# Performance work log

Measured on AMD Instinct MI355X. Metric: run time of the kernel, lower is better.

## Reference

```python
import jax, jax.numpy as jnp
import numpy as np

WINDOW_SIZE = 11
C1 = 0.01 ** 2
C2 = 0.03 ** 2


def _box_filter(x, ws):
    # x: [B,1,H,W]; uniform box filter, zero padding (== torch conv2d pad=ws//2)
    k = jnp.full((1, 1, ws, ws), 1.0 / (ws * ws), dtype=x.dtype)
    pad = ws // 2
    return jax.lax.conv_general_dilated(
        x, k, window_strides=(1, 1), padding=[(pad, pad), (pad, pad)],
        dimension_numbers=('NCHW', 'OIHW', 'NCHW'))


def setup_inputs() -> dict:
    key = jax.random.key(0)
    k1, k2 = jax.random.split(key)
    img1 = jax.random.uniform(k1, (64, 1, 512, 512), dtype=jnp.float32)
    img2 = jax.random.uniform(k2, (64, 1, 512, 512), dtype=jnp.float32)
    return {"img1": img1, "img2": img2}


def reference(img1, img2):
    ws = WINDOW_SIZE
    mu1 = _box_filter(img1, ws)
    mu2 = _box_filter(img2, ws)
    mu1_sq = mu1 * mu1
    mu2_sq = mu2 * mu2
    mu1_mu2 = mu1 * mu2
    sigma1_sq = _box_filter(img1 * img1, ws) - mu1_sq
    sigma2_sq = _box_filter(img2 * img2, ws) - mu2_sq
    sigma12 = _box_filter(img1 * img2, ws) - mu1_mu2
    ssim_map = ((2 * mu1_mu2 + C1) * (2 * sigma12 + C2)) / (
        (mu1_sq + mu2_sq + C1) * (sigma1_sq + sigma2_sq + C2))
    return 1.0 - jnp.mean(ssim_map)
```

## Files before the change

### kernel.cpp

```cpp
#include <hip/hip_runtime.h>


#define IMG_H 512
#define IMG_W 512
#define N_IMG 64
#define STRIP 16
#define NTHREADS 128
#define SSZ 528
#define QSZ 132
#define ROWSZ (SSZ + QSZ)

__global__ __launch_bounds__(NTHREADS) void ssim_kernel(const float* __restrict__ img1,
                                                        const float* __restrict__ img2,
                                                        float* __restrict__ ws) {
    __shared__ __align__(16) float V[2][4][ROWSZ];
    __shared__ float wsum[2];
    const int t = threadIdx.x;
    const int b = blockIdx.y;
    const int r0 = blockIdx.x * STRIP;
    const float* __restrict__ p1 = img1 + (size_t)b * (IMG_H * IMG_W);
    const float* __restrict__ p2 = img2 + (size_t)b * (IMG_H * IMG_W);

    for (int i = t; i < 2 * 4 * ROWSZ; i += NTHREADS) (&V[0][0][0])[i] = 0.0f;

    const int c4 = 4 * t;
    float cs[4][4];
#pragma unroll
    for (int ch = 0; ch < 4; ++ch)
#pragma unroll
        for (int j = 0; j < 4; ++j) cs[ch][j] = 0.0f;

    auto addrow = [&](int r) {
        float4 x = *(const float4*)(p1 + (size_t)r * IMG_W + c4);
        float4 y = *(const float4*)(p2 + (size_t)r * IMG_W + c4);
        float xs[4] = {x.x, x.y, x.z, x.w}, ys[4] = {y.x, y.y, y.z, y.w};
#pragma unroll
        for (int j = 0; j < 4; ++j) {
            float u = xs[j] + ys[j], v = xs[j] - ys[j];
            cs[0][j] += u;                  cs[1][j] += v;
            cs[2][j] = fmaf(u, u, cs[2][j]); cs[3][j] = fmaf(v, v, cs[3][j]);
        }
    };

    float4 pax, pay, psx, psy;
    auto prefetch = [&](int rn) {
        if (rn >= r0 + STRIP) return;
        const int ra = rn + 5, rs = rn - 6;
        if (ra < IMG_H) {
            pax = *(const float4*)(p1 + (size_t)ra * IMG_W + c4);
            pay = *(const float4*)(p2 + (size_t)ra * IMG_W + c4);
        }
        if (rs >= 0) {
            psx = *(const float4*)(p1 + (size_t)rs * IMG_W + c4);
            psy = *(const float4*)(p2 + (size_t)rs * IMG_W + c4);
        }
    };
    auto consume = [&](int rn) {
        const int ra = rn + 5, rs = rn - 6;
        if (ra < IMG_H) {
            float xs[4] = {pax.x, pax.y, pax.z, pax.w};
            float ys[4] = {pay.x, pay.y, pay.z, pay.w};
#pragma unroll
            for (int j = 0; j < 4; ++j) {
                float u = xs[j] + ys[j], v = xs[j] - ys[j];
                cs[0][j] += u;                  cs[1][j] += v;
                cs[2][j] = fmaf(u, u, cs[2][j]); cs[3][j] = fmaf(v, v, cs[3][j]);
            }
        }
        if (rs >= 0) {
            float xs[4] = {psx.x, psx.y, psx.z, psx.w};
            float ys[4] = {psy.x, psy.y, psy.z, psy.w};
#pragma unroll
            for (int j = 0; j < 4; ++j) {
                float u = xs[j] + ys[j], v = xs[j] - ys[j];
                cs[0][j] -= u;                  cs[1][j] -= v;
                cs[2][j] = fmaf(-u, u, cs[2][j]); cs[3][j] = fmaf(-v, v, cs[3][j]);
            }
        }
    };
    auto writeSQ = [&](int p) {
#pragma unroll
        for (int ch = 0; ch < 4; ++ch) {
            *(float4*)&V[p][ch][8 + c4] =
                make_float4(cs[ch][0], cs[ch][1], cs[ch][2], cs[ch][3]);
            V[p][ch][SSZ + 2 + t] = (cs[ch][0] + cs[ch][1]) + (cs[ch][2] + cs[ch][3]);
        }
    };

    int offS[4][3], offQ[4][2];
#pragma unroll
    for (int k = 0; k < 4; ++k) {
        const int c = t + 128 * k;
        const int rho = c & 3;
        int e0, e1, e2;
        if (rho == 0)      { e0 = -5; e1 =  4; e2 =  5; }
        else if (rho == 1) { e0 =  3; e1 =  4; e2 =  5; }
        else if (rho == 2) { e0 = -5; e1 = -4; e2 = -3; }
        else               { e0 = -5; e1 = -4; e2 =  5; }
        offS[k][0] = c + 8 + e0; offS[k][1] = c + 8 + e1; offS[k][2] = c + 8 + e2;
        const int mlo = (c >> 2) + ((rho < 2) ? -1 : 0);
        offQ[k][0] = SSZ + 2 + mlo; offQ[k][1] = SSZ + 3 + mlo;
    }

    {
        int rlo = r0 - 5; if (rlo < 0) rlo = 0;
        const int rhi = r0 + 5;
        for (int r = rlo; r <= rhi; ++r) addrow(r);
    }
    __syncthreads();
    writeSQ(0);
    prefetch(r0 + 1);
    __syncthreads();

    constexpr float inv  = 1.0f / 121.0f;
    constexpr float inv2 = 0.5f / 121.0f;
    constexpr float C1c = 0.01f * 0.01f;
    constexpr float C2c = 0.03f * 0.03f;
    float acc = 0.0f;

    auto hphase = [&](int p) {
        const float* __restrict__ Vf = &V[p][0][0];
#pragma unroll
        for (int k = 0; k < 4; ++k) {
            float W[4];
#pragma unroll
            for (int ch = 0; ch < 4; ++ch) {
                const int base = ch * ROWSZ;
                W[ch] = ((Vf[base + offS[k][0]] + Vf[base + offS[k][1]]) +
                         (Vf[base + offS[k][2]] + Vf[base + offQ[k][0]])) +
                        Vf[base + offQ[k][1]];
            }
            float mu_u = W[0] * inv, mu_v = W[1] * inv;
            float uu = mu_u * mu_u, vv = mu_v * mu_v;
            float P = 0.5f * (uu + vv);
            float M = 0.5f * (uu - vv);
            float A = fmaf(W[2] + W[3], inv2, -P);
            float B = fmaf(W[2] - W[3], inv2, -M);
            float num = (M + C1c) * (B + C2c);
            float den = (P + C1c) * (A + C2c);
            acc += __fdividef(num, den);
        }
    };

    for (int i = 0; i < STRIP - 1; ++i) {
        hphase(i & 1);
        consume(r0 + i + 1);
        prefetch(r0 + i + 2);
        writeSQ((i + 1) & 1);
        __syncthreads();
    }
    hphase((STRIP - 1) & 1);

#pragma unroll
    for (int off = 32; off > 0; off >>= 1) acc += __shfl_down(acc, off);
    if ((t & 63) == 0) wsum[t >> 6] = acc;
    __syncthreads();
    if (t == 0) atomicAdd(ws, wsum[0] + wsum[1]);
}

__global__ void ssim_finalize(const float* __restrict__ ws, float* __restrict__ out) {
    constexpr float inv_n = 1.0f / (float)((size_t)N_IMG * IMG_H * IMG_W);
    out[0] = 1.0f - ws[0] * inv_n;
}

extern "C" void kernel_launch(void* const* d_in, const int* in_sizes, int n_in,
                              void* d_out, int out_size, void* d_ws, size_t ws_size,
                              hipStream_t stream) {
    const float* img1 = (const float*)d_in[0];
    const float* img2 = (const float*)d_in[1];
    float* out = (float*)d_out;
    float* ws = (float*)d_ws;

    hipMemsetAsync(ws, 0, sizeof(float), stream);

    dim3 grid(IMG_H / STRIP, N_IMG);
    ssim_kernel<<<grid, NTHREADS, 0, stream>>>(img1, img2, ws);
    ssim_finalize<<<1, 1, 0, stream>>>(ws, out);
}
```

Measured before the change: 191.8 us.

## Use single-wavefront blocks with one LDS buffer and no block barriers

Shrinks each block to one 64-thread wavefront that covers the full 512-column row, with each thread owning two float4 column groups. Halves the strip height and drops the double-buffered LDS. It also removes every __syncthreads, relying on in-wavefront ordering of LDS writes and reads, and does the final reduction with a single atomic per wave. The aim is to cut barrier stalls and raise occupancy through more, smaller blocks. In exchange, the shorter strips reload more halo rows per output row, and correctness now depends on wavefront-synchronous LDS ordering.

Result: slower. 642.4 us (+235.0%).

```diff
diff --git a/kernel.cpp b/kernel.cpp
--- a/kernel.cpp
+++ b/kernel.cpp
@@ -4,35 +4,33 @@
 #define IMG_H 512
 #define IMG_W 512
 #define N_IMG 64
-#define STRIP 16
-#define NTHREADS 128
+#define STRIP 8
+#define NTHREADS 64
 #define SSZ 528
 #define QSZ 132
 #define ROWSZ (SSZ + QSZ)
 
-__global__ __launch_bounds__(NTHREADS) void ssim_kernel(const float* __restrict__ img1,
-                                                        const float* __restrict__ img2,
-                                                        float* __restrict__ ws) {
-    __shared__ __align__(16) float V[2][4][ROWSZ];
-    __shared__ float wsum[2];
+__global__ __launch_bounds__(NTHREADS, 4) void ssim_kernel(const float* __restrict__ img1,
+                                                           const float* __restrict__ img2,
+                                                           float* __restrict__ ws) {
+    __shared__ __align__(16) float V[4][ROWSZ];
     const int t = threadIdx.x;
     const int b = blockIdx.y;
     const int r0 = blockIdx.x * STRIP;
     const float* __restrict__ p1 = img1 + (size_t)b * (IMG_H * IMG_W);
     const float* __restrict__ p2 = img2 + (size_t)b * (IMG_H * IMG_W);
 
-    for (int i = t; i < 2 * 4 * ROWSZ; i += NTHREADS) (&V[0][0][0])[i] = 0.0f;
+    for (int i = t; i < 4 * ROWSZ; i += NTHREADS) (&V[0][0])[i] = 0.0f;
 
-    const int c4 = 4 * t;
-    float cs[4][4];
+    const int c4a = 4 * t;
+    const int c4b = 4 * t + 256;
+    float csA[4][4], csB[4][4];
 #pragma unroll
     for (int ch = 0; ch < 4; ++ch)
 #pragma unroll
-        for (int j = 0; j < 4; ++j) cs[ch][j] = 0.0f;
+        for (int j = 0; j < 4; ++j) { csA[ch][j] = 0.0f; csB[ch][j] = 0.0f; }
 
-    auto addrow = [&](int r) {
-        float4 x = *(const float4*)(p1 + (size_t)r * IMG_W + c4);
-        float4 y = *(const float4*)(p2 + (size_t)r * IMG_W + c4);
+    auto addQ = [&](float (&cs)[4][4], float4 x, float4 y) {
         float xs[4] = {x.x, x.y, x.z, x.w}, ys[4] = {y.x, y.y, y.z, y.w};
 #pragma unroll
         for (int j = 0; j < 4; ++j) {
@@ -41,94 +39,93 @@
             cs[2][j] = fmaf(u, u, cs[2][j]); cs[3][j] = fmaf(v, v, cs[3][j]);
         }
     };
+    auto subQ = [&](float (&cs)[4][4], float4 x, float4 y) {
+        float xs[4] = {x.x, x.y, x.z, x.w}, ys[4] = {y.x, y.y, y.z, y.w};
+#pragma unroll
+        for (int j = 0; j < 4; ++j) {
+            float u = xs[j] + ys[j], v = xs[j] - ys[j];
+            cs[0][j] -= u;                  cs[1][j] -= v;
+            cs[2][j] = fmaf(-u, u, cs[2][j]); cs[3][j] = fmaf(-v, v, cs[3][j]);
+        }
+    };
 
-    float4 pax, pay, psx, psy;
+#pragma unroll
+    for (int dr = -5; dr <= 5; ++dr) {
+        const int r = r0 + dr;
+        if (r >= 0) {
+            float4 xa = *(const float4*)(p1 + (size_t)r * IMG_W + c4a);
+            float4 ya = *(const float4*)(p2 + (size_t)r * IMG_W + c4a);
+            float4 xb = *(const float4*)(p1 + (size_t)r * IMG_W + c4b);
+            float4 yb = *(const float4*)(p2 + (size_t)r * IMG_W + c4b);
+            addQ(csA, xa, ya); addQ(csB, xb, yb);
+        }
+    }
+
+    float4 paxA, payA, paxB, payB, psxA, psyA, psxB, psyB;
     auto prefetch = [&](int rn) {
         if (rn >= r0 + STRIP) return;
         const int ra = rn + 5, rs = rn - 6;
         if (ra < IMG_H) {
-            pax = *(const float4*)(p1 + (size_t)ra * IMG_W + c4);
-            pay = *(const float4*)(p2 + (size_t)ra * IMG_W + c4);
+            paxA = *(const float4*)(p1 + (size_t)ra * IMG_W + c4a);
+            payA = *(const float4*)(p2 + (size_t)ra * IMG_W + c4a);
+            paxB = *(const float4*)(p1 + (size_t)ra * IMG_W + c4b);
+            payB = *(const float4*)(p2 + (size_t)ra * IMG_W + c4b);
         }
         if (rs >= 0) {
-            psx = *(const float4*)(p1 + (size_t)rs * IMG_W + c4);
-            psy = *(const float4*)(p2 + (size_t)rs * IMG_W + c4);
+            psxA = *(const float4*)(p1 + (size_t)rs * IMG_W + c4a);
+            psyA = *(const float4*)(p2 + (size_t)rs * IMG_W + c4a);
+            psxB = *(const float4*)(p1 + (size_t)rs * IMG_W + c4b);
+            psyB = *(const float4*)(p2 + (size_t)rs * IMG_W + c4b);
         }
     };
     auto consume = [&](int rn) {
         const int ra = rn + 5, rs = rn - 6;
-        if (ra < IMG_H) {
-            float xs[4] = {pax.x, pax.y, pax.z, pax.w};
-            float ys[4] = {pay.x, pay.y, pay.z, pay.w};
-#pragma unroll
-            for (int j = 0; j < 4; ++j) {
-                float u = xs[j] + ys[j], v = xs[j] - ys[j];
-                cs[0][j] += u;                  cs[1][j] += v;
-                cs[2][j] = fmaf(u, u, cs[2][j]); cs[3][j] = fmaf(v, v, cs[3][j]);
-            }
-        }
-        if (rs >= 0) {
-            float xs[4] = {psx.x, psx.y, psx.z, psx.w};
-            float ys[4] = {psy.x, psy.y, psy.z, psy.w};
-#pragma unroll
-            for (int j = 0; j < 4; ++j) {
-                float u = xs[j] + ys[j], v = xs[j] - ys[j];
-                cs[0][j] -= u;                  cs[1][j] -= v;
-                cs[2][j] = fmaf(-u, u, cs[2][j]); cs[3][j] = fmaf(-v, v, cs[3][j]);
-            }
-        }
+        if (ra < IMG_H) { addQ(csA, paxA, payA); addQ(csB, paxB, payB); }
+        if (rs >= 0)    { subQ(csA, psxA, psyA); subQ(csB, psxB, psyB); }
     };
-    auto writeSQ = [&](int p) {
+
+    auto writeSQ = [&]() {
 #pragma unroll
         for (int ch = 0; ch < 4; ++ch) {
-            *(float4*)&V[p][ch][8 + c4] =
-                make_float4(cs[ch][0], cs[ch][1], cs[ch][2], cs[ch][3]);
-            V[p][ch][SSZ + 2 + t] = (cs[ch][0] + cs[ch][1]) + (cs[ch][2] + cs[ch][3]);
+            *(float4*)&V[ch][8 + c4a] =
+                make_float4(csA[ch][0], csA[ch][1], csA[ch][2], csA[ch][3]);
+            *(float4*)&V[ch][8 + c4b] =
+                make_float4(csB[ch][0], csB[ch][1], csB[ch][2], csB[ch][3]);
+            V[ch][SSZ + 2 + t]      = (csA[ch][0] + csA[ch][1]) + (csA[ch][2] + csA[ch][3]);
+            V[ch][SSZ + 2 + 64 + t] = (csB[ch][0] + csB[ch][1]) + (csB[ch][2] + csB[ch][3]);
         }
     };
 
-    int offS[4][3], offQ[4][2];
-#pragma unroll
-    for (int k = 0; k < 4; ++k) {
-        const int c = t + 128 * k;
-        const int rho = c & 3;
+    int sOff[3], qOff[2];
+    {
+        const int rho = t & 3;
         int e0, e1, e2;
         if (rho == 0)      { e0 = -5; e1 =  4; e2 =  5; }
         else if (rho == 1) { e0 =  3; e1 =  4; e2 =  5; }
         else if (rho == 2) { e0 = -5; e1 = -4; e2 = -3; }
         else               { e0 = -5; e1 = -4; e2 =  5; }
-        offS[k][0] = c + 8 + e0; offS[k][1] = c + 8 + e1; offS[k][2] = c + 8 + e2;
-        const int mlo = (c >> 2) + ((rho < 2) ? -1 : 0);
-        offQ[k][0] = SSZ + 2 + mlo; offQ[k][1] = SSZ + 3 + mlo;
+        sOff[0] = t + 8 + e0; sOff[1] = t + 8 + e1; sOff[2] = t + 8 + e2;
+        const int mlo = (t >> 2) + ((rho < 2) ? -1 : 0);
+        qOff[0] = SSZ + 2 + mlo; qOff[1] = SSZ + 3 + mlo;
     }
-
-    {
-        int rlo = r0 - 5; if (rlo < 0) rlo = 0;
-        const int rhi = r0 + 5;
-        for (int r = rlo; r <= rhi; ++r) addrow(r);
-    }
-    __syncthreads();
-    writeSQ(0);
-    prefetch(r0 + 1);
-    __syncthreads();
 
     constexpr float inv  = 1.0f / 121.0f;
     constexpr float inv2 = 0.5f / 121.0f;
     constexpr float C1c = 0.01f * 0.01f;
     constexpr float C2c = 0.03f * 0.03f;
     float acc = 0.0f;
+    const float* __restrict__ Vf = &V[0][0];
 
-    auto hphase = [&](int p) {
-        const float* __restrict__ Vf = &V[p][0][0];
+    auto hphase = [&]() {
 #pragma unroll
-        for (int k = 0; k < 4; ++k) {
+        for (int k = 0; k < 8; ++k) {
             float W[4];
 #pragma unroll
             for (int ch = 0; ch < 4; ++ch) {
                 const int base = ch * ROWSZ;
-                W[ch] = ((Vf[base + offS[k][0]] + Vf[base + offS[k][1]]) +
-                         (Vf[base + offS[k][2]] + Vf[base + offQ[k][0]])) +
-                        Vf[base + offQ[k][1]];
+                W[ch] = ((Vf[base + sOff[0] + 64 * k] + Vf[base + sOff[1] + 64 * k]) +
+                         (Vf[base + sOff[2] + 64 * k] + Vf[base + qOff[0] + 16 * k])) +
+                        Vf[base + qOff[1] + 16 * k];
             }
             float mu_u = W[0] * inv, mu_v = W[1] * inv;
             float uu = mu_u * mu_u, vv = mu_v * mu_v;
@@ -142,20 +139,19 @@
         }
     };
 
+    writeSQ();
+    prefetch(r0 + 1);
     for (int i = 0; i < STRIP - 1; ++i) {
-        hphase(i & 1);
+        hphase();
         consume(r0 + i + 1);
         prefetch(r0 + i + 2);
-        writeSQ((i + 1) & 1);
-        __syncthreads();
+        writeSQ();
     }
-    hphase((STRIP - 1) & 1);
+    hphase();
 
 #pragma unroll
     for (int off = 32; off > 0; off >>= 1) acc += __shfl_down(acc, off);
-    if ((t & 63) == 0) wsum[t >> 6] = acc;
-    __syncthreads();
-    if (t == 0) atomicAdd(ws, wsum[0] + wsum[1]);
+    if (t == 0) atomicAdd(ws, acc);
 }
 
 __global__ void ssim_finalize(const float* __restrict__ ws, float* __restrict__ out) {
```
